# Performance work log

Hardware: AMD Instinct MI355X
Metric: run time of the kernel (lower is better)

## Reference

```python
import jax, jax.numpy as jnp
import numpy as np

EPS_LN = 1e-5
EPS_NORM = 1e-12


def _layernorm(h, g, b):
    mu = jnp.mean(h, axis=-1, keepdims=True)
    var = jnp.mean((h - mu) ** 2, axis=-1, keepdims=True)
    return (h - mu) * jax.lax.rsqrt(var + EPS_LN) * g + b


def _l2norm(h):
    n = jnp.linalg.norm(h, axis=-1, keepdims=True)
    return h / jnp.maximum(n, EPS_NORM)


def setup_inputs() -> dict:
    key = jax.random.key(0)
    ks = jax.random.split(key, 6)
    B, S, D = 8, 4096, 1024
    A, C, dc = 16, 8, 64      # n_anchors, n_comp, d_comp
    apc = A // C              # anchors per compartment = 2
    x = jax.random.normal(ks[0], (B, S, D), jnp.float32)
    anchors = jax.random.normal(ks[1], (A, D), jnp.float32)  # normalized inside forward
    ln_g = jnp.ones((D,), jnp.float32)
    ln_b = jnp.zeros((D,), jnp.float32)
    W1 = jax.random.normal(ks[2], (C, apc, 2 * dc), jnp.float32) / np.sqrt(apc)
    b1 = jnp.zeros((C, 2 * dc), jnp.float32)
    W2 = jax.random.normal(ks[3], (C, 2 * dc, dc), jnp.float32) / np.sqrt(2 * dc)
    b2 = jnp.zeros((C, dc), jnp.float32)
    cg = jnp.ones((C, dc), jnp.float32)
    cb = jnp.zeros((C, dc), jnp.float32)
    Wp = jax.random.normal(ks[4], (C * dc, D), jnp.float32) / np.sqrt(C * dc)
    bp = jnp.zeros((D,), jnp.float32)
    gate = jnp.full((D,), -3.0, jnp.float32)  # gate_init = -3.0
    return dict(x=x, anchors=anchors, ln_g=ln_g, ln_b=ln_b, W1=W1, b1=b1,
                W2=W2, b2=b2, cg=cg, cb=cb, Wp=Wp, bp=bp, gate=gate)


def reference(x, anchors, ln_g, ln_b, W1, b1, W2, b2, cg, cb, Wp, bp, gate):
    B, S, D = x.shape
    C, apc, _ = W1.shape
    dc = W2.shape[-1]
    # LayerNorm then L2-normalize each token
    h = _l2norm(_layernorm(x.reshape(B * S, D), ln_g, ln_b))  # (N, D)
    a = _l2norm(anchors)                                      # (A, D)
    tri = 1.0 - h @ a.T                                       # (N, A)
    # asgn = arange(A) % C -> comp k reads columns [k, k+C, ...]
    g = tri.reshape(-1, apc, C)                               # g[:, j, k] = tri[:, j*C + k]
    u = jnp.einsum('nak,kae->nke', g, W1) + b1                # (N, C, 2*dc)
    u = jnp.square(jnp.maximum(u, 0.0))                       # squared ReLU
    y = jnp.einsum('nke,ked->nkd', u, W2) + b2                # (N, C, dc)
    y = _layernorm(y, cg, cb)                                 # per-comp LayerNorm over dc
    y = y.reshape(-1, C * dc)                                 # concat comps in order
    update = (y @ Wp + bp).reshape(B, S, D)
    return x + jax.nn.sigmoid(gate) * update
```

## Files before the change

### kernel.cpp

```cpp
#include <hip/hip_runtime.h>
#include <hip/hip_bf16.h>

#define DIM 1024
#define NANCH 16
#define NCOMP 8
#define DC 64
#define DC2 128
#define EPS_LN 1e-5f
#define EPS_NORM 1e-12f

typedef __bf16 bf16x8 __attribute__((ext_vector_type(8)));
typedef float f32x4 __attribute__((ext_vector_type(4)));

template <int CTRL>
__device__ __forceinline__ float rr_add(float v) {
  return v + __int_as_float(__builtin_amdgcn_update_dpp(
                 0, __float_as_int(v), CTRL, 0xF, 0xF, true));
}
__device__ __forceinline__ float rowsum16(float v) {
  v = rr_add<0x121>(v);
  v = rr_add<0x122>(v);
  v = rr_add<0x124>(v);
  v = rr_add<0x128>(v);
  return v;
}
__device__ __forceinline__ float wavesum64(float v) {
  v = rowsum16(v);
  v += __shfl_xor(v, 16);
  v += __shfl_xor(v, 32);
  return v;
}

__device__ __forceinline__ void gload16(const __hip_bfloat16* g, __hip_bfloat16* l) {
  __builtin_amdgcn_global_load_lds(
      (const __attribute__((address_space(1))) unsigned int*)g,
      (__attribute__((address_space(3))) unsigned int*)l, 16, 0, 0);
}

__global__ __launch_bounds__(256) void kprepall(
    const float* __restrict__ anchors, const float* __restrict__ Wp,
    const float* __restrict__ W2, __hip_bfloat16* __restrict__ WpT,
    __hip_bfloat16* __restrict__ W2B, __hip_bfloat16* __restrict__ AnB) {
  __shared__ float smem[64 * 65 + 16];
  int b = blockIdx.x, t = threadIdx.x;

  if (b < 16) {
    int a = b, lane = t & 63, wid = t >> 6;
    float v[4]; float ss = 0.f;
#pragma unroll
    for (int i = 0; i < 4; i++) {
      v[i] = anchors[a * DIM + t + 256 * i];
      ss += v[i] * v[i];
    }
    for (int off = 32; off; off >>= 1) ss += __shfl_down(ss, off);
    if (lane == 0) smem[4160 + wid] = ss;
    __syncthreads();
    float inv = 1.f / fmaxf(sqrtf(smem[4160] + smem[4161] + smem[4162] + smem[4163]),
                            EPS_NORM);
#pragma unroll
    for (int i = 0; i < 4; i++) smem[t + 256 * i] = v[i] * inv;
    __syncthreads();
#pragma unroll
    for (int q = 0; q < 4; q++) {
      int idx = t * 4 + q;
      int ks = idx >> 5, hi = (idx >> 3) & 3, j = idx & 7;
      AnB[ks * 512 + (hi * 16 + a) * 8 + j] = __float2bfloat16(smem[idx]);
    }
  } else if (b < 144) {
    int bidx = b - 16, bj = bidx & 15, bk = bidx >> 4;
    int tx = t & 63, ty = t >> 6;
#pragma unroll
    for (int i = 0; i < 16; i++) {
      int r = ty + 4 * i;
      smem[r * 65 + tx] = Wp[(size_t)(bk * 64 + r) * DIM + bj * 64 + tx];
    }
    __syncthreads();
#pragma unroll
    for (int i = 0; i < 16; i++) {
      int r = ty + 4 * i;
      WpT[(size_t)(bj * 64 + r) * 512 + bk * 64 + tx] =
          __float2bfloat16(smem[tx * 65 + r]);
    }
  } else {
    int id = (b - 144) * 256 + t;
    int j = id & 7, lane = (id >> 3) & 63, ks = (id >> 9) & 3,
        nt = (id >> 11) & 3, k = id >> 13;
    int e = ks * 32 + (lane >> 4) * 8 + j;
    int n = nt * 16 + (lane & 15);
    W2B[id] = __float2bfloat16(W2[k * (DC2 * DC) + e * DC + n]);
  }
}

#define LDA_H 1032
__global__ __launch_bounds__(256, 7) void ktoken(
    const float* __restrict__ x, const __hip_bfloat16* __restrict__ AnB,
    const float* __restrict__ ln_g, const float* __restrict__ ln_b,
    const float* __restrict__ W1, const float* __restrict__ b1,
    const __hip_bfloat16* __restrict__ W2B, const float* __restrict__ b2,
    const float* __restrict__ cg, const float* __restrict__ cb,
    __hip_bfloat16* __restrict__ yout) {
  int t = threadIdx.x;
  int lane = t & 63, w = t >> 6;
  int l15 = lane & 15, quad = lane >> 4;
  int n0 = blockIdx.x * 8;

  __shared__ __hip_bfloat16 hu[8 * LDA_H];
  __shared__ float tri_s[8 * 16];
  __shared__ float part[4 * 32 * 4];

  float gv[16], bv[16];
#pragma unroll
  for (int i = 0; i < 4; i++) {
    f32x4 g4 = *(const f32x4*)(&ln_g[i * 256 + lane * 4]);
    f32x4 b4 = *(const f32x4*)(&ln_b[i * 256 + lane * 4]);
#pragma unroll
    for (int j = 0; j < 4; j++) { gv[i * 4 + j] = g4[j]; bv[i * 4 + j] = b4[j]; }
  }
#pragma unroll
  for (int it = 0; it < 2; it++) {
    int tok = w * 2 + it;
    const float* xr = x + (size_t)(n0 + tok) * DIM;
    float xv[16], s = 0.f, s2 = 0.f;
#pragma unroll
    for (int i = 0; i < 4; i++) {
      f32x4 v4 = *(const f32x4*)(&xr[i * 256 + lane * 4]);
#pragma unroll
      for (int j = 0; j < 4; j++) {
        float v = v4[j];
        xv[i * 4 + j] = v; s += v; s2 += v * v;
      }
    }
    s = wavesum64(s);
    s2 = wavesum64(s2);
    float mu = s * (1.f / DIM);
    float rstd = rsqrtf(s2 * (1.f / DIM) - mu * mu + EPS_LN);
    float ss = 0.f;
#pragma unroll
    for (int i = 0; i < 16; i++) {
      float h = (xv[i] - mu) * rstd * gv[i] + bv[i];
      xv[i] = h; ss += h * h;
    }
    ss = wavesum64(ss);
    float inv = 1.f / fmaxf(sqrtf(ss), EPS_NORM);
#pragma unroll
    for (int i = 0; i < 4; i++) {
      union { uint2 u; __hip_bfloat16 h[4]; } pk;
#pragma unroll
      for (int j = 0; j < 4; j++) pk.h[j] = __float2bfloat16(xv[i * 4 + j] * inv);
      *(uint2*)(&hu[tok * LDA_H + i * 256 + lane * 4]) = pk.u;
    }
  }
  __syncthreads();

  {
    f32x4 tacc = {0.f, 0.f, 0.f, 0.f};
    int ar = l15 & 7;
#pragma unroll
    for (int ks = w * 8; ks < w * 8 + 8; ks++) {
      bf16x8 afr = *(const bf16x8*)(&hu[ar * LDA_H + ks * 32 + quad * 8]);
      bf16x8 bfr = *(const bf16x8*)(&AnB[ks * 512 + lane * 8]);
      tacc = __builtin_amdgcn_mfma_f32_16x16x32_bf16(afr, bfr, tacc, 0, 0, 0);
    }
    if (quad < 2) *(f32x4*)(&part[(w * 32 + (lane & 31)) * 4]) = tacc;
  }
  __syncthreads();
  if (t < 128) {
    int ln = t & 31, rg = t >> 5;
    float v = part[(0 * 32 + ln) * 4 + rg] + part[(1 * 32 + ln) * 4 + rg] +
              part[(2 * 32 + ln) * 4 + rg] + part[(3 * 32 + ln) * 4 + rg];
    int m = (ln >> 4) * 4 + rg, a = ln & 15;
    tri_s[m * 16 + a] = 1.f - v;
  }
  __syncthreads();

  {
    int k = t >> 5;
    int e0 = (t * 4) & 127;
    f32x4 w1a = *(const f32x4*)(&W1[k * 256 + e0]);
    f32x4 w1b = *(const f32x4*)(&W1[k * 256 + 128 + e0]);
    f32x4 b1v = *(const f32x4*)(&b1[k * 128 + e0]);
#pragma unroll
    for (int tok = 0; tok < 8; tok++) {
      float t0 = tri_s[tok * 16 + k], t1 = tri_s[tok * 16 + 8 + k];
      union { unsigned long long u; __hip_bfloat16 h[4]; } pk;
#pragma unroll
      for (int j = 0; j < 4; j++) {
        float uu = t0 * w1a[j] + t1 * w1b[j] + b1v[j];
        uu = fmaxf(uu, 0.f);
        pk.h[j] = __float2bfloat16(uu * uu);
      }
      *(unsigned long long*)(&hu[tok * LDA_H + t * 4]) = pk.u;
    }
  }
  __syncthreads();

#pragma unroll
  for (int kc = 0; kc < 2; kc++) {
    int k = w * 2 + kc;
    int ar = l15 & 7;
    bf16x8 afr[4];
#pragma unroll
    for (int ks = 0; ks < 4; ks++)
      afr[ks] = *(const bf16x8*)(&hu[ar * LDA_H + k * 128 + ks * 32 + quad * 8]);
    f32x4 acc[4] = {{0,0,0,0},{0,0,0,0},{0,0,0,0},{0,0,0,0}};
#pragma unroll
    for (int nt = 0; nt < 4; nt++) {
#pragma unroll
      for (int ks = 0; ks < 4; ks++) {
        bf16x8 bfr = *(const bf16x8*)(&W2B[(size_t)(((k * 4 + nt) * 4 + ks)) * 512 + lane * 8]);
        acc[nt] = __builtin_amdgcn_mfma_f32_16x16x32_bf16(afr[ks], bfr, acc[nt], 0, 0, 0);
      }
    }
    float vals[4][4], s1[4] = {0,0,0,0}, s2[4] = {0,0,0,0};
#pragma unroll
    for (int nt = 0; nt < 4; nt++) {
      float b2v = b2[k * 64 + nt * 16 + l15];
#pragma unroll
      for (int r = 0; r < 4; r++) {
        float v = acc[nt][r] + b2v;
        vals[nt][r] = v; s1[r] += v; s2[r] += v * v;
      }
    }
#pragma unroll
    for (int r = 0; r < 4; r++) {
      s1[r] = rowsum16(s1[r]);
      s2[r] = rowsum16(s2[r]);
    }
#pragma unroll
    for (int r = 0; r < 4; r++) {
      float mu = s1[r] * (1.f / DC);
      float rs = rsqrtf(s2[r] * (1.f / DC) - mu * mu + EPS_LN);
      int tokrow = quad * 4 + r;
      if (tokrow < 8) {
#pragma unroll
        for (int nt = 0; nt < 4; nt++) {
          int d = nt * 16 + l15;
          float yn = (vals[nt][r] - mu) * rs * cg[k * 64 + d] + cb[k * 64 + d];
          yout[(size_t)(n0 + tokrow) * 512 + k * 64 + d] = __float2bfloat16(yn);
        }
      }
    }
  }
}

__global__ __launch_bounds__(256, 4) void kgemm(
    const __hip_bfloat16* __restrict__ Y, const __hip_bfloat16* __restrict__ WpT,
    const float* __restrict__ x, const float* __restrict__ bp,
    const float* __restrict__ gate, float* __restrict__ out) {
  __shared__ alignas(16) __hip_bfloat16 As[128 * 64];
  __shared__ alignas(16) __hip_bfloat16 Bs[128 * 64];
  int t = threadIdx.x, lane = t & 63, wid = t >> 6;
  int bm = blockIdx.x, bj = blockIdx.y;
  int wm = (wid >> 1) * 64, wj = (wid & 1) * 64;
  int l15 = lane & 15, quad = lane >> 4;

  f32x4 acc[4][4] = {};

  int srow[4], scol[4];
#pragma unroll
  for (int it = 0; it < 4; it++) {
    int byteo = it * 4096 + t * 16;
    int row = byteo >> 7, colb = byteo & 127;
    srow[it] = row;
    scol[it] = (colb ^ ((row & 7) << 4)) >> 1;
  }

  for (int kt = 0; kt < 8; kt++) {
    int k0 = kt * 64;
#pragma unroll
    for (int it = 0; it < 4; it++) {
      gload16(Y + (size_t)(bm * 128 + srow[it]) * 512 + k0 + scol[it],
              As + (it * 4096 + t * 16) / 2);
      gload16(WpT + (size_t)(bj * 128 + srow[it]) * 512 + k0 + scol[it],
              Bs + (it * 4096 + t * 16) / 2);
    }
    __syncthreads();
#pragma unroll
    for (int kk = 0; kk < 64; kk += 32) {
      bf16x8 af[4], bfr[4];
#pragma unroll
      for (int i = 0; i < 4; i++) {
        int ra = wm + i * 16 + l15, rb = wj + i * 16 + l15;
        int cb2 = (kk + quad * 8) * 2;
        af[i]  = *(const bf16x8*)((const char*)As + ra * 128 + (cb2 ^ ((ra & 7) << 4)));
        bfr[i] = *(const bf16x8*)((const char*)Bs + rb * 128 + (cb2 ^ ((rb & 7) << 4)));
      }
#pragma unroll
      for (int i = 0; i < 4; i++)
#pragma unroll
        for (int j = 0; j < 4; j++)
          acc[i][j] = __builtin_amdgcn_mfma_f32_16x16x32_bf16(af[i], bfr[j], acc[i][j], 0, 0, 0);
    }
    __syncthreads();
  }

  float sg[4], bpv[4];
#pragma unroll
  for (int j = 0; j < 4; j++) {
    int gc = bj * 128 + wj + j * 16 + l15;
    sg[j] = 1.f / (1.f + expf(-gate[gc]));
    bpv[j] = bp[gc];
  }
#pragma unroll
  for (int i = 0; i < 4; i++) {
#pragma unroll
    for (int j = 0; j < 4; j++) {
      int gc = bj * 128 + wj + j * 16 + l15;
#pragma unroll
      for (int r = 0; r < 4; r++) {
        int gr = bm * 128 + wm + i * 16 + quad * 4 + r;
        size_t idx = (size_t)gr * DIM + gc;
        out[idx] = x[idx] + sg[j] * (acc[i][j][r] + bpv[j]);
      }
    }
  }
}

extern "C" void kernel_launch(void* const* d_in, const int* in_sizes, int n_in,
                              void* d_out, int out_size, void* d_ws, size_t ws_size,
                              hipStream_t stream) {
  const float* x       = (const float*)d_in[0];
  const float* anchors = (const float*)d_in[1];
  const float* ln_g    = (const float*)d_in[2];
  const float* ln_b    = (const float*)d_in[3];
  const float* W1      = (const float*)d_in[4];
  const float* b1      = (const float*)d_in[5];
  const float* W2      = (const float*)d_in[6];
  const float* b2      = (const float*)d_in[7];
  const float* cg      = (const float*)d_in[8];
  const float* cb      = (const float*)d_in[9];
  const float* Wp      = (const float*)d_in[10];
  const float* bp      = (const float*)d_in[11];
  const float* gate    = (const float*)d_in[12];

  int N = in_sizes[0] / DIM;

  char* w = (char*)d_ws;
  size_t off = 0;
  __hip_bfloat16* WpT = (__hip_bfloat16*)(w + off);  off += 1 << 20;
  __hip_bfloat16* W2B = (__hip_bfloat16*)(w + off);  off += 128 << 10;
  __hip_bfloat16* AnB = (__hip_bfloat16*)(w + off);  off += 32 << 10;
  __hip_bfloat16* Yb  = (__hip_bfloat16*)(w + off);

  kprepall<<<400, 256, 0, stream>>>(anchors, Wp, W2, WpT, W2B, AnB);
  ktoken<<<N / 8, 256, 0, stream>>>(x, AnB, ln_g, ln_b, W1, b1, W2B, b2, cg, cb, Yb);
  kgemm<<<dim3(N / 128, DIM / 128), 256, 0, stream>>>(Yb, WpT, x, bp, gate,
                                                      (float*)d_out);
}
```

Baseline: 340.9 us.

## Split token kernel into tri-computation and compartment-MLP kernels

The fused per-token kernel is split in two. The first kernel does LayerNorm, L2 norm and the anchor product, then writes tri to a global scratch buffer. The second kernel reads tri and runs the squared-ReLU MLP, the W2 MFMA and the per-compartment LayerNorm. This may let each kernel get better occupancy or scheduling, but it adds a global round trip and an extra launch.

After: 358.4 us. 1.05x slower.

```diff
diff --git a/kernel.cpp b/kernel.cpp
--- a/kernel.cpp
+++ b/kernel.cpp
@@ -31,7 +31,7 @@
   return v;
 }
 
-__device__ __forceinline__ void gload16(const __hip_bfloat16* g, __hip_bfloat16* l) {
+__device__ __forceinline__ void gload16(const void* g, void* l) {
   __builtin_amdgcn_global_load_lds(
       (const __attribute__((address_space(1))) unsigned int*)g,
       (__attribute__((address_space(3))) unsigned int*)l, 16, 0, 0);
@@ -92,20 +92,16 @@
 }
 
 #define LDA_H 1032
-__global__ __launch_bounds__(256, 7) void ktoken(
+__global__ __launch_bounds__(256, 7) void kt1(
     const float* __restrict__ x, const __hip_bfloat16* __restrict__ AnB,
     const float* __restrict__ ln_g, const float* __restrict__ ln_b,
-    const float* __restrict__ W1, const float* __restrict__ b1,
-    const __hip_bfloat16* __restrict__ W2B, const float* __restrict__ b2,
-    const float* __restrict__ cg, const float* __restrict__ cb,
-    __hip_bfloat16* __restrict__ yout) {
+    float* __restrict__ triG) {
   int t = threadIdx.x;
   int lane = t & 63, w = t >> 6;
   int l15 = lane & 15, quad = lane >> 4;
   int n0 = blockIdx.x * 8;
 
-  __shared__ __hip_bfloat16 hu[8 * LDA_H];
-  __shared__ float tri_s[8 * 16];
+  __shared__ __hip_bfloat16 hs[8 * LDA_H];
   __shared__ float part[4 * 32 * 4];
 
   float gv[16], bv[16];
@@ -147,7 +143,7 @@
       union { uint2 u; __hip_bfloat16 h[4]; } pk;
 #pragma unroll
       for (int j = 0; j < 4; j++) pk.h[j] = __float2bfloat16(xv[i * 4 + j] * inv);
-      *(uint2*)(&hu[tok * LDA_H + i * 256 + lane * 4]) = pk.u;
+      *(uint2*)(&hs[tok * LDA_H + i * 256 + lane * 4]) = pk.u;
     }
   }
   __syncthreads();
@@ -157,7 +153,7 @@
     int ar = l15 & 7;
 #pragma unroll
     for (int ks = w * 8; ks < w * 8 + 8; ks++) {
-      bf16x8 afr = *(const bf16x8*)(&hu[ar * LDA_H + ks * 32 + quad * 8]);
+      bf16x8 afr = *(const bf16x8*)(&hs[ar * LDA_H + ks * 32 + quad * 8]);
       bf16x8 bfr = *(const bf16x8*)(&AnB[ks * 512 + lane * 8]);
       tacc = __builtin_amdgcn_mfma_f32_16x16x32_bf16(afr, bfr, tacc, 0, 0, 0);
     }
@@ -169,8 +165,24 @@
     float v = part[(0 * 32 + ln) * 4 + rg] + part[(1 * 32 + ln) * 4 + rg] +
               part[(2 * 32 + ln) * 4 + rg] + part[(3 * 32 + ln) * 4 + rg];
     int m = (ln >> 4) * 4 + rg, a = ln & 15;
-    tri_s[m * 16 + a] = 1.f - v;
-  }
+    triG[(size_t)(n0 + m) * 16 + a] = 1.f - v;
+  }
+}
+
+__global__ __launch_bounds__(256, 7) void kt2(
+    const float* __restrict__ triG, const float* __restrict__ W1,
+    const float* __restrict__ b1, const __hip_bfloat16* __restrict__ W2B,
+    const float* __restrict__ b2, const float* __restrict__ cg,
+    const float* __restrict__ cb, __hip_bfloat16* __restrict__ yout) {
+  int t = threadIdx.x;
+  int lane = t & 63, w = t >> 6;
+  int l15 = lane & 15, quad = lane >> 4;
+  int n0 = blockIdx.x * 8;
+
+  __shared__ __hip_bfloat16 us[8 * LDA_H];
+  __shared__ float tri_s[8 * 16];
+
+  if (t < 128) tri_s[t] = triG[(size_t)n0 * 16 + t];
   __syncthreads();
 
   {
@@ -189,7 +201,7 @@
         uu = fmaxf(uu, 0.f);
         pk.h[j] = __float2bfloat16(uu * uu);
       }
-      *(unsigned long long*)(&hu[tok * LDA_H + t * 4]) = pk.u;
+      *(unsigned long long*)(&us[tok * LDA_H + t * 4]) = pk.u;
     }
   }
   __syncthreads();
@@ -201,7 +213,7 @@
     bf16x8 afr[4];
 #pragma unroll
     for (int ks = 0; ks < 4; ks++)
-      afr[ks] = *(const bf16x8*)(&hu[ar * LDA_H + k * 128 + ks * 32 + quad * 8]);
+      afr[ks] = *(const bf16x8*)(&us[ar * LDA_H + k * 128 + ks * 32 + quad * 8]);
     f32x4 acc[4] = {{0,0,0,0},{0,0,0,0},{0,0,0,0},{0,0,0,0}};
 #pragma unroll
     for (int nt = 0; nt < 4; nt++) {
@@ -340,10 +352,12 @@
   __hip_bfloat16* WpT = (__hip_bfloat16*)(w + off);  off += 1 << 20;
   __hip_bfloat16* W2B = (__hip_bfloat16*)(w + off);  off += 128 << 10;
   __hip_bfloat16* AnB = (__hip_bfloat16*)(w + off);  off += 32 << 10;
+  float* triG         = (float*)(w + off);           off += (size_t)N * 16 * 4;
   __hip_bfloat16* Yb  = (__hip_bfloat16*)(w + off);
 
   kprepall<<<400, 256, 0, stream>>>(anchors, Wp, W2, WpT, W2B, AnB);
-  ktoken<<<N / 8, 256, 0, stream>>>(x, AnB, ln_g, ln_b, W1, b1, W2B, b2, cg, cb, Yb);
+  kt1<<<N / 8, 256, 0, stream>>>(x, AnB, ln_g, ln_b, triG);
+  kt2<<<N / 8, 256, 0, stream>>>(triG, W1, b1, W2B, b2, cg, cb, Yb);
   kgemm<<<dim3(N / 128, DIM / 128), 256, 0, stream>>>(Yb, WpT, x, bp, gate,
                                                       (float*)d_out);
 }
```
